# Kernel optimization log

Measured on AMD Instinct MI355X. Metric: run time of the kernel, lower is better.

The kernel has to match this reference:

```python
import jax, jax.numpy as jnp
import numpy as np

WINDOW_SIZES = (4, 8, 16, 32)


def setup_inputs() -> dict:
    key = jax.random.key(0)
    k1, k2 = jax.random.split(key)
    B, L, D = 128, 1024, 128
    sequence_emb = jax.random.normal(k1, (B, L, D), dtype=jnp.float32)
    mask = jax.random.randint(k2, (B, L), 0, 2, dtype=jnp.int32)
    return {"sequence_emb": sequence_emb, "mask": mask}


def reference(sequence_emb, mask):
    # sequence_emb: (B, L, D); mask: (B, L) int 0/1
    B, L, D = sequence_emb.shape
    m = mask.astype(sequence_emb.dtype)
    masked = sequence_emb * m[..., None]  # (B, L, D)
    # prefix sums with leading zero so window sum = cs[i+w] - cs[i]
    zero_v = jnp.zeros((B, 1, D), dtype=sequence_emb.dtype)
    cs = jnp.concatenate([zero_v, jnp.cumsum(masked, axis=1)], axis=1)  # (B, L+1, D)
    zero_m = jnp.zeros((B, 1), dtype=sequence_emb.dtype)
    cm = jnp.concatenate([zero_m, jnp.cumsum(m, axis=1)], axis=1)  # (B, L+1)
    outs = []
    for w in WINDOW_SIZES:
        if L < w:
            continue
        win_sum = cs[:, w:, :] - cs[:, :-w, :]          # (B, L-w+1, D)
        win_len = jnp.clip(cm[:, w:] - cm[:, :-w], 1.0)  # (B, L-w+1)
        outs.append(win_sum / win_len[..., None])
    return jnp.concatenate(outs, axis=1)  # (B, sum(L-w+1), D)
```

## Files before the change

kernel.cpp:

```cpp
#include <hip/hip_runtime.h>


namespace {
constexpr int kB    = 128;
constexpr int kL    = 1024;
constexpr int kD    = 128;
constexpr int kD4   = kD / 4;
constexpr int TILE  = 64;
constexpr int HALO  = 32;
constexpr int ROWS  = TILE + HALO;
constexpr int ROUT  = 4040;
constexpr int OFF4  = 0;
constexpr int OFF8  = 1021;
constexpr int OFF16 = 2038;
constexpr int OFF32 = 3047;
}

typedef float v4f __attribute__((ext_vector_type(4)));

__device__ __forceinline__ void nt_store(float4* p, const float4& v) {
    v4f x;
    x.x = v.x; x.y = v.y; x.z = v.z; x.w = v.w;
    __builtin_nontemporal_store(x, reinterpret_cast<v4f*>(p));
}
__device__ __forceinline__ float4 nt_load(const float4* p) {
    v4f x = __builtin_nontemporal_load(reinterpret_cast<const v4f*>(p));
    return make_float4(x.x, x.y, x.z, x.w);
}

__device__ __forceinline__ void acc4(float4& a, const float4& x) {
    a.x += x.x; a.y += x.y; a.z += x.z; a.w += x.w;
}
__device__ __forceinline__ void slide4(float4& a, const float4& xin, const float4& xout) {
    a.x += xin.x - xout.x; a.y += xin.y - xout.y;
    a.z += xin.z - xout.z; a.w += xin.w - xout.w;
}
__device__ __forceinline__ float4 scale4(const float4& v, float s) {
    return make_float4(v.x * s, v.y * s, v.z * s, v.w * s);
}

__global__ __launch_bounds__(256)
void msse_kernel(const float* __restrict__ emb,
                 const int*   __restrict__ mask,
                 float*       __restrict__ out) {
    __shared__ float4 s_data[ROWS * kD4];
    __shared__ float  s_mask[ROWS];
    __shared__ float  s_inv[4][TILE];

    const int b  = blockIdx.y;
    const int i0 = blockIdx.x * TILE;
    const int t  = threadIdx.x;

    const float4* gsrc = reinterpret_cast<const float4*>(emb) + (size_t)b * kL * kD4;
    #pragma unroll
    for (int k = 0; k < (ROWS * kD4) / 256; ++k) {
        const int f    = t + k * 256;
        const int row  = f >> 5;
        const int grow = i0 + row;
        float4 v = make_float4(0.f, 0.f, 0.f, 0.f);
        float  m = 0.f;
        if (grow < kL) {
            m = (float)mask[b * kL + grow];
            v = nt_load(gsrc + grow * kD4 + (f & 31));
            v.x *= m; v.y *= m; v.z *= m; v.w *= m;
        }
        s_data[f] = v;
        if ((f & 31) == 0) s_mask[row] = m;
    }
    __syncthreads();

    if (t < TILE) {
        float c = 0.f, c4 = 0.f, c8 = 0.f, c16 = 0.f;
        #pragma unroll
        for (int j = 0; j < 32; ++j) {
            c += s_mask[t + j];
            if (j == 3)  c4  = c;
            if (j == 7)  c8  = c;
            if (j == 15) c16 = c;
        }
        s_inv[0][t] = 1.f / fmaxf(c4,  1.f);
        s_inv[1][t] = 1.f / fmaxf(c8,  1.f);
        s_inv[2][t] = 1.f / fmaxf(c16, 1.f);
        s_inv[3][t] = 1.f / fmaxf(c,   1.f);
    }
    __syncthreads();

    const int lane  = t & 31;
    const int strip = t >> 5;
    const int base  = strip * 8;

    const float4* col = s_data + lane;

    float4 s4, s8, s16, s32;
    {
        float4 a  = make_float4(0.f, 0.f, 0.f, 0.f);
        float4 t4 = a, t8 = a, t16 = a;
        #pragma unroll
        for (int j = 0; j < 32; ++j) {
            acc4(a, col[(base + j) * kD4]);
            if (j == 3)  t4  = a;
            if (j == 7)  t8  = a;
            if (j == 15) t16 = a;
        }
        s4 = t4; s8 = t8; s16 = t16; s32 = a;
    }

    float4* outb = reinterpret_cast<float4*>(out) + (size_t)b * ROUT * kD4 + lane;

    #pragma unroll
    for (int p = 0; p < 8; ++p) {
        const int il = base + p;
        const int i  = i0 + il;

        if (i <= kL - 4)  nt_store(outb + (OFF4  + i) * kD4, scale4(s4,  s_inv[0][il]));
        if (i <= kL - 8)  nt_store(outb + (OFF8  + i) * kD4, scale4(s8,  s_inv[1][il]));
        if (i <= kL - 16) nt_store(outb + (OFF16 + i) * kD4, scale4(s16, s_inv[2][il]));
        if (i <= kL - 32) nt_store(outb + (OFF32 + i) * kD4, scale4(s32, s_inv[3][il]));

        const float4 x0 = col[(il)      * kD4];
        const float4 xa = col[(il + 4)  * kD4];
        const float4 xb = col[(il + 8)  * kD4];
        const float4 xc = col[(il + 16) * kD4];
        const float4 xd = col[(il + 32) * kD4];
        slide4(s4,  xa, x0);
        slide4(s8,  xb, x0);
        slide4(s16, xc, x0);
        slide4(s32, xd, x0);
    }
}

extern "C" void kernel_launch(void* const* d_in, const int* in_sizes, int n_in,
                              void* d_out, int out_size, void* d_ws, size_t ws_size,
                              hipStream_t stream) {
    const float* emb  = (const float*)d_in[0];
    const int*   mask = (const int*)d_in[1];
    float*       out  = (float*)d_out;

    dim3 grid((kL + TILE - 1) / TILE, kB);
    dim3 block(256);
    msse_kernel<<<grid, block, 0, stream>>>(emb, mask, out);
}
```

Baseline: 313.2 us.

## Split D into halves per block, remap blocks across XCDs, raise occupancy

Each block now handles half of the feature dimension, which doubles the block count and halves shared memory per block. Each thread computes 4 output rows instead of 8. A 1D grid is remapped so that consecutive logical tiles land on the same XCD, aiming for better L2 locality, and launch bounds request 6 waves per EU for higher occupancy. Non-temporal loads are swapped for plain loads. The halo rows are now loaded twice as often relative to output rows, which adds redundant input traffic.

```diff
diff --git a/kernel.cpp b/kernel.cpp
--- a/kernel.cpp
+++ b/kernel.cpp
@@ -6,6 +6,7 @@
 constexpr int kL    = 1024;
 constexpr int kD    = 128;
 constexpr int kD4   = kD / 4;
+constexpr int kDH4  = kD4 / 2;
 constexpr int TILE  = 64;
 constexpr int HALO  = 32;
 constexpr int ROWS  = TILE + HALO;
@@ -14,6 +15,10 @@
 constexpr int OFF8  = 1021;
 constexpr int OFF16 = 2038;
 constexpr int OFF32 = 3047;
+constexpr int NTILE = kL / TILE;
+constexpr int NXCD  = 8;
+constexpr int NBLK  = kB * 2 * NTILE;
+constexpr int CPX   = NBLK / NXCD;
 }
 
 typedef float v4f __attribute__((ext_vector_type(4)));
@@ -22,10 +27,6 @@
     v4f x;
     x.x = v.x; x.y = v.y; x.z = v.z; x.w = v.w;
     __builtin_nontemporal_store(x, reinterpret_cast<v4f*>(p));
-}
-__device__ __forceinline__ float4 nt_load(const float4* p) {
-    v4f x = __builtin_nontemporal_load(reinterpret_cast<const v4f*>(p));
-    return make_float4(x.x, x.y, x.z, x.w);
 }
 
 __device__ __forceinline__ void acc4(float4& a, const float4& x) {
@@ -39,33 +40,39 @@
     return make_float4(v.x * s, v.y * s, v.z * s, v.w * s);
 }
 
-__global__ __launch_bounds__(256)
+__global__ __launch_bounds__(256, 6)
 void msse_kernel(const float* __restrict__ emb,
                  const int*   __restrict__ mask,
                  float*       __restrict__ out) {
-    __shared__ float4 s_data[ROWS * kD4];
+    __shared__ float4 s_data[ROWS * kDH4];
     __shared__ float  s_mask[ROWS];
     __shared__ float  s_inv[4][TILE];
 
-    const int b  = blockIdx.y;
-    const int i0 = blockIdx.x * TILE;
-    const int t  = threadIdx.x;
+    const int hid  = blockIdx.x;
+    const int l    = (hid & (NXCD - 1)) * CPX + (hid >> 3);
+    const int tile = l & (NTILE - 1);
+    const int bh   = l >> 4;
+    const int b    = bh >> 1;
+    const int half = bh & 1;
+    const int i0   = tile * TILE;
+    const int t    = threadIdx.x;
 
-    const float4* gsrc = reinterpret_cast<const float4*>(emb) + (size_t)b * kL * kD4;
+    const float4* gsrc = reinterpret_cast<const float4*>(emb)
+                       + (size_t)b * kL * kD4 + half * kDH4;
     #pragma unroll
-    for (int k = 0; k < (ROWS * kD4) / 256; ++k) {
+    for (int k = 0; k < (ROWS * kDH4) / 256; ++k) {
         const int f    = t + k * 256;
-        const int row  = f >> 5;
+        const int row  = f >> 4;
         const int grow = i0 + row;
         float4 v = make_float4(0.f, 0.f, 0.f, 0.f);
         float  m = 0.f;
         if (grow < kL) {
             m = (float)mask[b * kL + grow];
-            v = nt_load(gsrc + grow * kD4 + (f & 31));
+            v = gsrc[(size_t)grow * kD4 + (f & 15)];
             v.x *= m; v.y *= m; v.z *= m; v.w *= m;
         }
         s_data[f] = v;
-        if ((f & 31) == 0) s_mask[row] = m;
+        if ((f & 15) == 0) s_mask[row] = m;
     }
     __syncthreads();
 
@@ -85,9 +92,9 @@
     }
     __syncthreads();
 
-    const int lane  = t & 31;
-    const int strip = t >> 5;
-    const int base  = strip * 8;
+    const int lane  = t & 15;
+    const int strip = t >> 4;
+    const int base  = strip * 4;
 
     const float4* col = s_data + lane;
 
@@ -97,7 +104,7 @@
         float4 t4 = a, t8 = a, t16 = a;
         #pragma unroll
         for (int j = 0; j < 32; ++j) {
-            acc4(a, col[(base + j) * kD4]);
+            acc4(a, col[(base + j) * kDH4]);
             if (j == 3)  t4  = a;
             if (j == 7)  t8  = a;
             if (j == 15) t16 = a;
@@ -105,23 +112,24 @@
         s4 = t4; s8 = t8; s16 = t16; s32 = a;
     }
 
-    float4* outb = reinterpret_cast<float4*>(out) + (size_t)b * ROUT * kD4 + lane;
+    float4* outb = reinterpret_cast<float4*>(out)
+                 + (size_t)b * ROUT * kD4 + half * kDH4 + lane;
 
     #pragma unroll
-    for (int p = 0; p < 8; ++p) {
+    for (int p = 0; p < 4; ++p) {
         const int il = base + p;
         const int i  = i0 + il;
 
-        if (i <= kL - 4)  nt_store(outb + (OFF4  + i) * kD4, scale4(s4,  s_inv[0][il]));
-        if (i <= kL - 8)  nt_store(outb + (OFF8  + i) * kD4, scale4(s8,  s_inv[1][il]));
-        if (i <= kL - 16) nt_store(outb + (OFF16 + i) * kD4, scale4(s16, s_inv[2][il]));
-        if (i <= kL - 32) nt_store(outb + (OFF32 + i) * kD4, scale4(s32, s_inv[3][il]));
+        if (i <= kL - 4)  nt_store(outb + (size_t)(OFF4  + i) * kD4, scale4(s4,  s_inv[0][il]));
+        if (i <= kL - 8)  nt_store(outb + (size_t)(OFF8  + i) * kD4, scale4(s8,  s_inv[1][il]));
+        if (i <= kL - 16) nt_store(outb + (size_t)(OFF16 + i) * kD4, scale4(s16, s_inv[2][il]));
+        if (i <= kL - 32) nt_store(outb + (size_t)(OFF32 + i) * kD4, scale4(s32, s_inv[3][il]));
 
-        const float4 x0 = col[(il)      * kD4];
-        const float4 xa = col[(il + 4)  * kD4];
-        const float4 xb = col[(il + 8)  * kD4];
-        const float4 xc = col[(il + 16) * kD4];
-        const float4 xd = col[(il + 32) * kD4];
+        const float4 x0 = col[(il)      * kDH4];
+        const float4 xa = col[(il + 4)  * kDH4];
+        const float4 xb = col[(il + 8)  * kDH4];
+        const float4 xc = col[(il + 16) * kDH4];
+        const float4 xd = col[(il + 32) * kDH4];
         slide4(s4,  xa, x0);
         slide4(s8,  xb, x0);
         slide4(s16, xc, x0);
@@ -136,7 +144,7 @@
     const int*   mask = (const int*)d_in[1];
     float*       out  = (float*)d_out;
 
-    dim3 grid((kL + TILE - 1) / TILE, kB);
+    dim3 grid(NBLK);
     dim3 block(256);
     msse_kernel<<<grid, block, 0, stream>>>(emb, mask, out);
 }
```

Result: slower. 401.7 us (+28.3%).

## Drop LDS staging of embeddings and read rows directly from global memory

Applied to the files above, without the earlier changes.

Removes the shared-memory tile of masked embeddings. Each thread team now reads rows straight from global memory and applies the mask through FMAs during accumulation and sliding, with only the mask held in LDS. The block covers 128 positions with 16 per warp team, and launch bounds ask for 4 blocks per CU. This frees LDS and cuts the load-then-sync phase so occupancy can rise, but each row is read up to five times from global memory and relies on cache hits instead of one staged load.

```diff
diff --git a/kernel.cpp b/kernel.cpp
--- a/kernel.cpp
+++ b/kernel.cpp
@@ -6,14 +6,14 @@
 constexpr int kL    = 1024;
 constexpr int kD    = 128;
 constexpr int kD4   = kD / 4;
-constexpr int TILE  = 64;
-constexpr int HALO  = 32;
-constexpr int ROWS  = TILE + HALO;
 constexpr int ROUT  = 4040;
 constexpr int OFF4  = 0;
 constexpr int OFF8  = 1021;
 constexpr int OFF16 = 2038;
 constexpr int OFF32 = 3047;
+constexpr int BPOS  = 128;
+constexpr int TP    = 16;
+constexpr int NCH   = kL / BPOS;
 }
 
 typedef float v4f __attribute__((ext_vector_type(4)));
@@ -23,57 +23,44 @@
     x.x = v.x; x.y = v.y; x.z = v.z; x.w = v.w;
     __builtin_nontemporal_store(x, reinterpret_cast<v4f*>(p));
 }
-__device__ __forceinline__ float4 nt_load(const float4* p) {
-    v4f x = __builtin_nontemporal_load(reinterpret_cast<const v4f*>(p));
-    return make_float4(x.x, x.y, x.z, x.w);
+__device__ __forceinline__ float4 f4zero() { return make_float4(0.f, 0.f, 0.f, 0.f); }
+
+__device__ __forceinline__ void fma4(float4& a, const float4& x, float m) {
+    a.x = fmaf(x.x, m, a.x); a.y = fmaf(x.y, m, a.y);
+    a.z = fmaf(x.z, m, a.z); a.w = fmaf(x.w, m, a.w);
 }
-
-__device__ __forceinline__ void acc4(float4& a, const float4& x) {
-    a.x += x.x; a.y += x.y; a.z += x.z; a.w += x.w;
-}
-__device__ __forceinline__ void slide4(float4& a, const float4& xin, const float4& xout) {
-    a.x += xin.x - xout.x; a.y += xin.y - xout.y;
-    a.z += xin.z - xout.z; a.w += xin.w - xout.w;
+__device__ __forceinline__ void slide4m(float4& a, const float4& xi, float mi,
+                                        const float4& xo, float mo) {
+    a.x = fmaf(xi.x, mi, fmaf(-xo.x, mo, a.x));
+    a.y = fmaf(xi.y, mi, fmaf(-xo.y, mo, a.y));
+    a.z = fmaf(xi.z, mi, fmaf(-xo.z, mo, a.z));
+    a.w = fmaf(xi.w, mi, fmaf(-xo.w, mo, a.w));
 }
 __device__ __forceinline__ float4 scale4(const float4& v, float s) {
     return make_float4(v.x * s, v.y * s, v.z * s, v.w * s);
 }
 
-__global__ __launch_bounds__(256)
+__global__ __launch_bounds__(256, 4)
 void msse_kernel(const float* __restrict__ emb,
                  const int*   __restrict__ mask,
                  float*       __restrict__ out) {
-    __shared__ float4 s_data[ROWS * kD4];
-    __shared__ float  s_mask[ROWS];
-    __shared__ float  s_inv[4][TILE];
+    __shared__ float s_maskf[BPOS + 32];
+    __shared__ float s_inv[4][BPOS];
 
     const int b  = blockIdx.y;
-    const int i0 = blockIdx.x * TILE;
+    const int P0 = blockIdx.x * BPOS;
     const int t  = threadIdx.x;
 
-    const float4* gsrc = reinterpret_cast<const float4*>(emb) + (size_t)b * kL * kD4;
-    #pragma unroll
-    for (int k = 0; k < (ROWS * kD4) / 256; ++k) {
-        const int f    = t + k * 256;
-        const int row  = f >> 5;
-        const int grow = i0 + row;
-        float4 v = make_float4(0.f, 0.f, 0.f, 0.f);
-        float  m = 0.f;
-        if (grow < kL) {
-            m = (float)mask[b * kL + grow];
-            v = nt_load(gsrc + grow * kD4 + (f & 31));
-            v.x *= m; v.y *= m; v.z *= m; v.w *= m;
-        }
-        s_data[f] = v;
-        if ((f & 31) == 0) s_mask[row] = m;
+    if (t < BPOS + 32) {
+        const int row = P0 + t;
+        s_maskf[t] = (row < kL) ? (float)mask[b * kL + row] : 0.f;
     }
     __syncthreads();
-
-    if (t < TILE) {
+    if (t < BPOS) {
         float c = 0.f, c4 = 0.f, c8 = 0.f, c16 = 0.f;
         #pragma unroll
         for (int j = 0; j < 32; ++j) {
-            c += s_mask[t + j];
+            c += s_maskf[t + j];
             if (j == 3)  c4  = c;
             if (j == 7)  c8  = c;
             if (j == 15) c16 = c;
@@ -85,19 +72,22 @@
     }
     __syncthreads();
 
-    const int lane  = t & 31;
-    const int strip = t >> 5;
-    const int base  = strip * 8;
+    const int lane = t & 31;
+    const int team = t >> 5;
+    const int l0   = team * TP;
+    const int p0   = P0 + l0;
 
-    const float4* col = s_data + lane;
+    const float4* g = reinterpret_cast<const float4*>(emb)
+                    + (size_t)b * kL * kD4 + lane;
 
     float4 s4, s8, s16, s32;
     {
-        float4 a  = make_float4(0.f, 0.f, 0.f, 0.f);
-        float4 t4 = a, t8 = a, t16 = a;
+        float4 a = f4zero(), t4 = a, t8 = a, t16 = a;
         #pragma unroll
         for (int j = 0; j < 32; ++j) {
-            acc4(a, col[(base + j) * kD4]);
+            const int r = p0 + j;
+            const float4 x = (r < kL) ? g[(size_t)r * kD4] : f4zero();
+            fma4(a, x, s_maskf[l0 + j]);
             if (j == 3)  t4  = a;
             if (j == 7)  t8  = a;
             if (j == 15) t16 = a;
@@ -105,27 +95,32 @@
         s4 = t4; s8 = t8; s16 = t16; s32 = a;
     }
 
-    float4* outb = reinterpret_cast<float4*>(out) + (size_t)b * ROUT * kD4 + lane;
+    float4* ob = reinterpret_cast<float4*>(out) + (size_t)b * ROUT * kD4 + lane;
 
     #pragma unroll
-    for (int p = 0; p < 8; ++p) {
-        const int il = base + p;
-        const int i  = i0 + il;
+    for (int p = 0; p < TP; ++p) {
+        const int li = l0 + p;
+        const int i  = P0 + li;
 
-        if (i <= kL - 4)  nt_store(outb + (OFF4  + i) * kD4, scale4(s4,  s_inv[0][il]));
-        if (i <= kL - 8)  nt_store(outb + (OFF8  + i) * kD4, scale4(s8,  s_inv[1][il]));
-        if (i <= kL - 16) nt_store(outb + (OFF16 + i) * kD4, scale4(s16, s_inv[2][il]));
-        if (i <= kL - 32) nt_store(outb + (OFF32 + i) * kD4, scale4(s32, s_inv[3][il]));
+        if (i <= kL - 4)  nt_store(&ob[(size_t)(OFF4  + i) * kD4], scale4(s4,  s_inv[0][li]));
+        if (i <= kL - 8)  nt_store(&ob[(size_t)(OFF8  + i) * kD4], scale4(s8,  s_inv[1][li]));
+        if (i <= kL - 16) nt_store(&ob[(size_t)(OFF16 + i) * kD4], scale4(s16, s_inv[2][li]));
+        if (i <= kL - 32) nt_store(&ob[(size_t)(OFF32 + i) * kD4], scale4(s32, s_inv[3][li]));
 
-        const float4 x0 = col[(il)      * kD4];
-        const float4 xa = col[(il + 4)  * kD4];
-        const float4 xb = col[(il + 8)  * kD4];
-        const float4 xc = col[(il + 16) * kD4];
-        const float4 xd = col[(il + 32) * kD4];
-        slide4(s4,  xa, x0);
-        slide4(s8,  xb, x0);
-        slide4(s16, xc, x0);
-        slide4(s32, xd, x0);
+        const float4 x0 = g[(size_t)i * kD4];
+        const float4 xa = (i + 4  < kL) ? g[(size_t)(i + 4)  * kD4] : f4zero();
+        const float4 xb = (i + 8  < kL) ? g[(size_t)(i + 8)  * kD4] : f4zero();
+        const float4 xc = (i + 16 < kL) ? g[(size_t)(i + 16) * kD4] : f4zero();
+        const float4 xd = (i + 32 < kL) ? g[(size_t)(i + 32) * kD4] : f4zero();
+        const float m0 = s_maskf[li];
+        const float ma = s_maskf[li + 4];
+        const float mb = s_maskf[li + 8];
+        const float mc = s_maskf[li + 16];
+        const float md = s_maskf[li + 32];
+        slide4m(s4,  xa, ma, x0, m0);
+        slide4m(s8,  xb, mb, x0, m0);
+        slide4m(s16, xc, mc, x0, m0);
+        slide4m(s32, xd, md, x0, m0);
     }
 }
 
@@ -136,7 +131,7 @@
     const int*   mask = (const int*)d_in[1];
     float*       out  = (float*)d_out;
 
-    dim3 grid((kL + TILE - 1) / TILE, kB);
+    dim3 grid(NCH, kB);
     dim3 block(256);
     msse_kernel<<<grid, block, 0, stream>>>(emb, mask, out);
 }
```

After: 381.0 us. +21.6%, slower.
